# Kernel optimization log

Hardware: AMD Instinct MI355X
Metric: run time of the kernel (lower is better)

The kernel has to match this reference:

```python
import jax, jax.numpy as jnp
import numpy as np

N, P, T, H, W = 16, 16, 8, 224, 224


def setup_inputs() -> dict:
    key = jax.random.key(0)
    k1, k2 = jax.random.split(key)
    # binary {0,1} group masks (torch version takes LongTensor; only nonzero pattern matters)
    groups_pred = jax.random.randint(k1, (N, P, H, W), 0, 2).astype(jnp.float32)
    groups_true = jax.random.randint(k2, (N, T, H, W), 0, 2).astype(jnp.float32)
    return {"groups_pred": groups_pred, "groups_true": groups_true}


def reference(groups_pred, groups_true):
    # binarize, matching torch's .bool().long()
    Gp = (groups_pred != 0).astype(jnp.float32)  # (N,P,H,W)
    Gt = (groups_true != 0).astype(jnp.float32)  # (N,T,H,W)

    # pairwise intersection via batched GEMM over flattened HW
    inters = jnp.einsum('nphw,nthw->npt', Gp, Gt)          # (N,P,T)
    sp = Gp.sum(axis=(-1, -2))                              # (N,P)
    st = Gt.sum(axis=(-1, -2))                              # (N,T)
    # |A u B| = |A| + |B| - |A n B| for binary masks == clamp(A+B,0,1).sum()
    unions = sp[:, :, None] + st[:, None, :] - inters       # (N,P,T)

    ious = inters / unions
    ious = jnp.where(jnp.isfinite(ious), ious, 0.0)
    iou_maxs = ious.max(axis=-1)                            # (N,P)

    # weight each predicted mask by its best IoU, sum over P
    pred_aligns_sum = jnp.einsum('nphw,np->nhw', Gp, iou_maxs)  # (N,H,W)
    score = pred_aligns_sum / Gp.sum(axis=1)                    # (N,H,W)
    score = jnp.where(jnp.isfinite(score), score, 0.0)
    return score.mean(axis=(1, 2))                              # (N,)
```

## Files before the change

### kernel.cpp

```cpp
#include <hip/hip_runtime.h>

#define NN 16
#define PB 16
#define TB 8
#define HWPX 50176
#define WORDS 784
#define SGW 16
#define SGPP 49

typedef unsigned long long u64;
typedef u64 u64x2 __attribute__((ext_vector_type(2)));

__global__ void pack_kernel(const float* __restrict__ pred,
                            const float* __restrict__ truth,
                            u64* __restrict__ PP, u64* __restrict__ PT,
                            float* __restrict__ inters, float* __restrict__ sp,
                            float* __restrict__ st, float* __restrict__ out) {
    if (blockIdx.x == 0) {
        const int TOT = NN * PB * TB + NN * PB + NN * TB + NN;
        for (int i = threadIdx.x; i < TOT; i += blockDim.x) {
            if (i < NN * PB * TB) inters[i] = 0.f;
            else if (i < NN * PB * TB + NN * PB) sp[i - NN * PB * TB] = 0.f;
            else if (i < NN * PB * TB + NN * PB + NN * TB)
                st[i - NN * PB * TB - NN * PB] = 0.f;
            else out[i - NN * PB * TB - NN * PB - NN * TB] = 0.f;
        }
    }

    const int totalSG = (NN * PB + NN * TB) * SGPP;
    const int wavesPerBlock = blockDim.x >> 6;
    const int waveId = blockIdx.x * wavesPerBlock + (threadIdx.x >> 6);
    const int lane = threadIdx.x & 63;
    const int nWaves = gridDim.x * wavesPerBlock;

    for (int G = waveId; G < totalSG; G += nWaves) {
        const int plane = G / SGPP;
        const int s = G - plane * SGPP;
        const float* src;
        u64* dst;
        if (plane < NN * PB) {
            src = pred + (size_t)plane * HWPX;
            dst = PP + (size_t)plane * WORDS;
        } else {
            const int q = plane - NN * PB;
            src = truth + (size_t)q * HWPX;
            dst = PT + (size_t)q * WORDS;
        }
        const float* b = src + s * 1024 + lane * 4;
        const float4 v0 = *(const float4*)(b);
        const float4 v1 = *(const float4*)(b + 256);
        const float4 v2 = *(const float4*)(b + 512);
        const float4 v3 = *(const float4*)(b + 768);
        u64 w0 = __ballot(v0.x != 0.f), w1 = __ballot(v0.y != 0.f);
        u64 w2 = __ballot(v0.z != 0.f), w3 = __ballot(v0.w != 0.f);
        u64 w4 = __ballot(v1.x != 0.f), w5 = __ballot(v1.y != 0.f);
        u64 w6 = __ballot(v1.z != 0.f), w7 = __ballot(v1.w != 0.f);
        u64 w8 = __ballot(v2.x != 0.f), w9 = __ballot(v2.y != 0.f);
        u64 wa = __ballot(v2.z != 0.f), wb = __ballot(v2.w != 0.f);
        u64 wc = __ballot(v3.x != 0.f), wd = __ballot(v3.y != 0.f);
        u64 we = __ballot(v3.z != 0.f), wf = __ballot(v3.w != 0.f);
        if (lane == 0) {
            u64x2* d = (u64x2*)(dst + s * SGW);
            u64x2 t0 = {w0, w1};
            u64x2 t1 = {w2, w3};
            u64x2 t2 = {w4, w5};
            u64x2 t3 = {w6, w7};
            u64x2 t4 = {w8, w9};
            u64x2 t5 = {wa, wb};
            u64x2 t6 = {wc, wd};
            u64x2 t7 = {we, wf};
            d[0] = t0;
            d[1] = t1;
            d[2] = t2;
            d[3] = t3;
            d[4] = t4;
            d[5] = t5;
            d[6] = t6;
            d[7] = t7;
        }
    }
}

#define K2_SPLIT 56
#define K2_W (WORDS / K2_SPLIT)
__global__ void inters_kernel(const u64* __restrict__ PP,
                              const u64* __restrict__ PT,
                              float* __restrict__ inters,
                              float* __restrict__ sp, float* __restrict__ st) {
    const int n = blockIdx.x / K2_SPLIT;
    const int s = blockIdx.x % K2_SPLIT;
    const int p = threadIdx.x >> 3;
    const int t = threadIdx.x & 7;
    const u64* pp = PP + ((size_t)n * PB + p) * WORDS + s * K2_W;
    const u64* pt = PT + ((size_t)n * TB + t) * WORDS + s * K2_W;
    int acc = 0, accp = 0, acct = 0;
#pragma unroll
    for (int w = 0; w < K2_W; w += 2) {
        const u64x2 a = *(const u64x2*)(pp + w);
        const u64x2 b = *(const u64x2*)(pt + w);
        acc += __popcll(a[0] & b[0]) + __popcll(a[1] & b[1]);
        accp += __popcll(a[0]) + __popcll(a[1]);
        acct += __popcll(b[0]) + __popcll(b[1]);
    }
    atomicAdd(&inters[((size_t)n * PB + p) * TB + t], (float)acc);
    if (t == 0) atomicAdd(&sp[n * PB + p], (float)accp);
    if (p == 0) atomicAdd(&st[n * TB + t], (float)acct);
}

#define K3_CH 49
#define K3_W (WORDS / K3_CH)
__global__ void score_kernel(const u64* __restrict__ PP,
                             const float* __restrict__ inters,
                             const float* __restrict__ sp,
                             const float* __restrict__ st,
                             float* __restrict__ out) {
    const int n = blockIdx.x / K3_CH;
    const int c = blockIdx.x % K3_CH;
    __shared__ float ioumax_s[PB];
    __shared__ float redbuf[4];

    if (threadIdx.x < PB) {
        const int p = threadIdx.x;
        const float spv = sp[n * PB + p];
        float m = 0.f;
#pragma unroll
        for (int t = 0; t < TB; ++t) {
            const float iv = inters[((size_t)n * PB + p) * TB + t];
            const float un = spv + st[n * TB + t] - iv;
            const float iou = un > 0.f ? iv / un : 0.f;
            m = fmaxf(m, iou);
        }
        ioumax_s[p] = m;
    }
    __syncthreads();

    float wgt[PB];
#pragma unroll
    for (int p = 0; p < PB; ++p) wgt[p] = ioumax_s[p];

    const int lane = threadIdx.x & 63;
    const int wv = threadIdx.x >> 6;
    const int wbase = c * K3_W + wv * 4;
    float sum = 0.f;
#pragma unroll
    for (int i = 0; i < 2; ++i) {
        const int w = wbase + i * 2;
        float num0 = 0.f, den0 = 0.f, num1 = 0.f, den1 = 0.f;
#pragma unroll
        for (int p = 0; p < PB; ++p) {
            const u64x2 m = *(const u64x2*)(PP + ((size_t)n * PB + p) * WORDS + w);
            const float b0 = (float)(unsigned)((m[0] >> lane) & 1ull);
            const float b1 = (float)(unsigned)((m[1] >> lane) & 1ull);
            den0 += b0;
            num0 = fmaf(b0, wgt[p], num0);
            den1 += b1;
            num1 = fmaf(b1, wgt[p], num1);
        }
        sum += (den0 > 0.f ? num0 / den0 : 0.f) + (den1 > 0.f ? num1 / den1 : 0.f);
    }

#pragma unroll
    for (int off = 32; off > 0; off >>= 1) sum += __shfl_down(sum, off, 64);
    if (lane == 0) redbuf[wv] = sum;
    __syncthreads();
    if (threadIdx.x == 0) {
        const float tot = redbuf[0] + redbuf[1] + redbuf[2] + redbuf[3];
        atomicAdd(&out[n], tot * (1.0f / (float)HWPX));
    }
}

extern "C" void kernel_launch(void* const* d_in, const int* in_sizes, int n_in,
                              void* d_out, int out_size, void* d_ws, size_t ws_size,
                              hipStream_t stream) {
    const float* pred = (const float*)d_in[0];
    const float* truth = (const float*)d_in[1];
    float* out = (float*)d_out;

    u64* PP = (u64*)d_ws;
    u64* PT = PP + (size_t)NN * PB * WORDS;
    float* inters = (float*)(PT + (size_t)NN * TB * WORDS);
    float* sp = inters + NN * PB * TB;
    float* st = sp + NN * PB;

    pack_kernel<<<1176, 256, 0, stream>>>(pred, truth, PP, PT, inters, sp, st, out);
    inters_kernel<<<NN * K2_SPLIT, 128, 0, stream>>>(PP, PT, inters, sp, st);
    score_kernel<<<NN * K3_CH, 256, 0, stream>>>(PP, inters, sp, st, out);
}
```

Measured before the change: 119.2 us.

## Fuse intersection popcount into pred packing after separate truth packing

```diff
diff --git a/kernel.cpp b/kernel.cpp
--- a/kernel.cpp
+++ b/kernel.cpp
@@ -11,11 +11,10 @@
 typedef unsigned long long u64;
 typedef u64 u64x2 __attribute__((ext_vector_type(2)));
 
-__global__ void pack_kernel(const float* __restrict__ pred,
-                            const float* __restrict__ truth,
-                            u64* __restrict__ PP, u64* __restrict__ PT,
-                            float* __restrict__ inters, float* __restrict__ sp,
-                            float* __restrict__ st, float* __restrict__ out) {
+__global__ void packT_kernel(const float* __restrict__ truth,
+                             u64* __restrict__ PT,
+                             float* __restrict__ inters, float* __restrict__ sp,
+                             float* __restrict__ st, float* __restrict__ out) {
     if (blockIdx.x == 0) {
         const int TOT = NN * PB * TB + NN * PB + NN * TB + NN;
         for (int i = threadIdx.x; i < TOT; i += blockDim.x) {
@@ -27,26 +26,16 @@
         }
     }
 
-    const int totalSG = (NN * PB + NN * TB) * SGPP;
+    const int totalSG = NN * TB * SGPP;
     const int wavesPerBlock = blockDim.x >> 6;
     const int waveId = blockIdx.x * wavesPerBlock + (threadIdx.x >> 6);
     const int lane = threadIdx.x & 63;
     const int nWaves = gridDim.x * wavesPerBlock;
 
     for (int G = waveId; G < totalSG; G += nWaves) {
-        const int plane = G / SGPP;
-        const int s = G - plane * SGPP;
-        const float* src;
-        u64* dst;
-        if (plane < NN * PB) {
-            src = pred + (size_t)plane * HWPX;
-            dst = PP + (size_t)plane * WORDS;
-        } else {
-            const int q = plane - NN * PB;
-            src = truth + (size_t)q * HWPX;
-            dst = PT + (size_t)q * WORDS;
-        }
-        const float* b = src + s * 1024 + lane * 4;
+        const int q = G / SGPP;
+        const int s = G - q * SGPP;
+        const float* b = truth + (size_t)q * HWPX + s * 1024 + lane * 4;
         const float4 v0 = *(const float4*)(b);
         const float4 v1 = *(const float4*)(b + 256);
         const float4 v2 = *(const float4*)(b + 512);
@@ -60,51 +49,102 @@
         u64 wc = __ballot(v3.x != 0.f), wd = __ballot(v3.y != 0.f);
         u64 we = __ballot(v3.z != 0.f), wf = __ballot(v3.w != 0.f);
         if (lane == 0) {
-            u64x2* d = (u64x2*)(dst + s * SGW);
-            u64x2 t0 = {w0, w1};
-            u64x2 t1 = {w2, w3};
-            u64x2 t2 = {w4, w5};
-            u64x2 t3 = {w6, w7};
-            u64x2 t4 = {w8, w9};
-            u64x2 t5 = {wa, wb};
-            u64x2 t6 = {wc, wd};
-            u64x2 t7 = {we, wf};
-            d[0] = t0;
-            d[1] = t1;
-            d[2] = t2;
-            d[3] = t3;
-            d[4] = t4;
-            d[5] = t5;
-            d[6] = t6;
-            d[7] = t7;
-        }
-    }
-}
-
-#define K2_SPLIT 56
-#define K2_W (WORDS / K2_SPLIT)
-__global__ void inters_kernel(const u64* __restrict__ PP,
-                              const u64* __restrict__ PT,
-                              float* __restrict__ inters,
-                              float* __restrict__ sp, float* __restrict__ st) {
-    const int n = blockIdx.x / K2_SPLIT;
-    const int s = blockIdx.x % K2_SPLIT;
-    const int p = threadIdx.x >> 3;
-    const int t = threadIdx.x & 7;
-    const u64* pp = PP + ((size_t)n * PB + p) * WORDS + s * K2_W;
-    const u64* pt = PT + ((size_t)n * TB + t) * WORDS + s * K2_W;
-    int acc = 0, accp = 0, acct = 0;
-#pragma unroll
-    for (int w = 0; w < K2_W; w += 2) {
-        const u64x2 a = *(const u64x2*)(pp + w);
-        const u64x2 b = *(const u64x2*)(pt + w);
-        acc += __popcll(a[0] & b[0]) + __popcll(a[1] & b[1]);
-        accp += __popcll(a[0]) + __popcll(a[1]);
-        acct += __popcll(b[0]) + __popcll(b[1]);
-    }
-    atomicAdd(&inters[((size_t)n * PB + p) * TB + t], (float)acc);
-    if (t == 0) atomicAdd(&sp[n * PB + p], (float)accp);
-    if (p == 0) atomicAdd(&st[n * TB + t], (float)acct);
+            u64x2* d = (u64x2*)(PT + (size_t)q * WORDS + s * SGW);
+            u64x2 t0 = {w0, w1}; u64x2 t1 = {w2, w3};
+            u64x2 t2 = {w4, w5}; u64x2 t3 = {w6, w7};
+            u64x2 t4 = {w8, w9}; u64x2 t5 = {wa, wb};
+            u64x2 t6 = {wc, wd}; u64x2 t7 = {we, wf};
+            d[0] = t0; d[1] = t1; d[2] = t2; d[3] = t3;
+            d[4] = t4; d[5] = t5; d[6] = t6; d[7] = t7;
+        }
+    }
+}
+
+__global__ void packP_kernel(const float* __restrict__ pred,
+                             const u64* __restrict__ PT,
+                             u64* __restrict__ PP,
+                             float* __restrict__ inters, float* __restrict__ sp,
+                             float* __restrict__ st) {
+    __shared__ u64 predw_s[4][SGW];
+    const int wavesPerBlock = blockDim.x >> 6;
+    const int wv = threadIdx.x >> 6;
+    const int lane = threadIdx.x & 63;
+    const int waveId = blockIdx.x * wavesPerBlock + wv;
+    const int nWaves = gridDim.x * wavesPerBlock;
+    const int totalSG = NN * PB * SGPP;
+
+    const int w = lane & 15;
+    const int tq = lane >> 4;
+
+    for (int G = waveId; G < totalSG; G += nWaves) {
+        const int ph = G / SGPP;
+        const int s = G - ph * SGPP;
+        const int n = ph >> 4;
+        const int p = ph & 15;
+
+        const float* b = pred + (size_t)ph * HWPX + s * 1024 + lane * 4;
+        const float4 v0 = *(const float4*)(b);
+        const float4 v1 = *(const float4*)(b + 256);
+        const float4 v2 = *(const float4*)(b + 512);
+        const float4 v3 = *(const float4*)(b + 768);
+        u64 w0 = __ballot(v0.x != 0.f), w1 = __ballot(v0.y != 0.f);
+        u64 w2 = __ballot(v0.z != 0.f), w3 = __ballot(v0.w != 0.f);
+        u64 w4 = __ballot(v1.x != 0.f), w5 = __ballot(v1.y != 0.f);
+        u64 w6 = __ballot(v1.z != 0.f), w7 = __ballot(v1.w != 0.f);
+        u64 w8 = __ballot(v2.x != 0.f), w9 = __ballot(v2.y != 0.f);
+        u64 wa = __ballot(v2.z != 0.f), wb = __ballot(v2.w != 0.f);
+        u64 wc = __ballot(v3.x != 0.f), wd = __ballot(v3.y != 0.f);
+        u64 we = __ballot(v3.z != 0.f), wf = __ballot(v3.w != 0.f);
+
+        if (lane == 0) {
+            u64x2* d = (u64x2*)(PP + (size_t)ph * WORDS + s * SGW);
+            u64x2 t0 = {w0, w1}; u64x2 t1 = {w2, w3};
+            u64x2 t2 = {w4, w5}; u64x2 t3 = {w6, w7};
+            u64x2 t4 = {w8, w9}; u64x2 t5 = {wa, wb};
+            u64x2 t6 = {wc, wd}; u64x2 t7 = {we, wf};
+            d[0] = t0; d[1] = t1; d[2] = t2; d[3] = t3;
+            d[4] = t4; d[5] = t5; d[6] = t6; d[7] = t7;
+            int spv = __popcll(w0) + __popcll(w1) + __popcll(w2) + __popcll(w3) +
+                      __popcll(w4) + __popcll(w5) + __popcll(w6) + __popcll(w7) +
+                      __popcll(w8) + __popcll(w9) + __popcll(wa) + __popcll(wb) +
+                      __popcll(wc) + __popcll(wd) + __popcll(we) + __popcll(wf);
+            atomicAdd(&sp[ph], (float)spv);
+            u64* ls = predw_s[wv];
+            ls[0] = w0; ls[1] = w1; ls[2] = w2; ls[3] = w3;
+            ls[4] = w4; ls[5] = w5; ls[6] = w6; ls[7] = w7;
+            ls[8] = w8; ls[9] = w9; ls[10] = wa; ls[11] = wb;
+            ls[12] = wc; ls[13] = wd; ls[14] = we; ls[15] = wf;
+        }
+        const u64 pw = predw_s[wv][w];
+
+        const u64* ptb = PT + ((size_t)n * TB) * WORDS + s * SGW + w;
+        const u64 pt0 = ptb[(size_t)tq * WORDS];
+        const u64 pt1 = ptb[(size_t)(tq + 4) * WORDS];
+        int i0 = __popcll(pw & pt0);
+        int i1 = __popcll(pw & pt1);
+#pragma unroll
+        for (int off = 1; off < 16; off <<= 1) {
+            i0 += __shfl_xor(i0, off, 64);
+            i1 += __shfl_xor(i1, off, 64);
+        }
+        if (w == 0) {
+            atomicAdd(&inters[ph * TB + tq], (float)i0);
+            atomicAdd(&inters[ph * TB + tq + 4], (float)i1);
+        }
+        if (p == 0) {
+            int c0 = __popcll(pt0);
+            int c1 = __popcll(pt1);
+#pragma unroll
+            for (int off = 1; off < 16; off <<= 1) {
+                c0 += __shfl_xor(c0, off, 64);
+                c1 += __shfl_xor(c1, off, 64);
+            }
+            if (w == 0) {
+                atomicAdd(&st[n * TB + tq], (float)c0);
+                atomicAdd(&st[n * TB + tq + 4], (float)c1);
+            }
+        }
+    }
 }
 
 #define K3_CH 49
@@ -182,7 +222,7 @@
     float* sp = inters + NN * PB * TB;
     float* st = sp + NN * PB;
 
-    pack_kernel<<<1176, 256, 0, stream>>>(pred, truth, PP, PT, inters, sp, st, out);
-    inters_kernel<<<NN * K2_SPLIT, 128, 0, stream>>>(PP, PT, inters, sp, st);
+    packT_kernel<<<784, 256, 0, stream>>>(truth, PT, inters, sp, st, out);
+    packP_kernel<<<1568, 256, 0, stream>>>(pred, PT, PP, inters, sp, st);
     score_kernel<<<NN * K3_CH, 256, 0, stream>>>(PP, inters, sp, st, out);
 }
```

Result: slower. 146.0 us (+22.5%).
